# Optimization experiments

Hardware: AMD Instinct MI355X
Metric: run time of the kernel (lower is better)

## Reference

```python
import jax, jax.numpy as jnp
import numpy as np

C_S, C_Z, C_H = 384, 128, 128
EPS = 0.001      # norm-divisor eps (module's self.eps)
LN_EPS = 1e-5    # nn.LayerNorm default eps


def setup_inputs() -> dict:
    key = jax.random.key(0)
    ks = jax.random.split(key, 8)
    sc_in = 1.0 / np.sqrt(C_S)
    sc_out = 1.0 / np.sqrt(2 * C_H)
    return {
        "s1": jax.random.normal(ks[0], (1, 512, C_S), dtype=jnp.float32),
        "s2": jax.random.normal(ks[1], (1, 512, C_S), dtype=jnp.float32),
        "W1": jax.random.normal(ks[2], (C_H, C_S), dtype=jnp.float32) * sc_in,
        "b1": jnp.zeros((C_H,), dtype=jnp.float32),
        "W2": jax.random.normal(ks[3], (C_H, C_S), dtype=jnp.float32) * sc_in,
        "b2": jnp.zeros((C_H,), dtype=jnp.float32),
        "gamma": jnp.ones((C_H,), dtype=jnp.float32),
        "beta": jnp.zeros((C_H,), dtype=jnp.float32),
        "Wout": jax.random.normal(ks[4], (C_Z, 2 * C_H), dtype=jnp.float32) * sc_out,
        "bout": jnp.zeros((C_Z,), dtype=jnp.float32),
    }


def _layer_norm(x, gamma, beta):
    mu = jnp.mean(x, axis=-1, keepdims=True)
    var = jnp.mean(jnp.square(x - mu), axis=-1, keepdims=True)
    return (x - mu) * jax.lax.rsqrt(var + LN_EPS) * gamma + beta


def reference(s1, s2, W1, b1, W2, b2, gamma, beta, Wout, bout):
    # project + layernorm: [B, N, c_h], [B, M, c_h]
    a = _layer_norm(jnp.einsum('bns,hs->bnh', s1, W1) + b1, gamma, beta)
    b = _layer_norm(jnp.einsum('bms,hs->bmh', s2, W2) + b2, gamma, beta)
    n, m = a.shape[1], b.shape[1]
    # pairwise outer-concat: [B, N, M, 2*c_h]
    cmct = jnp.concatenate([
        jnp.broadcast_to(a[:, :, None, :], (a.shape[0], n, m, a.shape[-1])),
        jnp.broadcast_to(b[:, None, :, :], (b.shape[0], n, m, b.shape[-1])),
    ], axis=-1)
    cmct = cmct / (EPS + n * m)
    # linear out: [B, N, M, c_z]
    return jnp.einsum('bnmh,zh->bnmz', cmct, Wout) + bout
```

## Files before the change

### kernel.cpp

```cpp
#include <hip/hip_runtime.h>

#define C_S 384
#define C_H 128
#define NROWS 512
#define R 2

typedef float f4 __attribute__((ext_vector_type(4)));

__global__ __launch_bounds__(256, 4) void proj_ln_out(
    const float* __restrict__ s1, const float* __restrict__ s2,
    const float* __restrict__ W1, const float* __restrict__ b1,
    const float* __restrict__ W2, const float* __restrict__ b2,
    const float* __restrict__ gamma, const float* __restrict__ beta,
    const float* __restrict__ Wout, const float* __restrict__ bout,
    float* __restrict__ u, float* __restrict__ v)
{
    const int bid = blockIdx.x;
    const int nb_side = NROWS / R;
    const bool isA = bid < nb_side;
    const int r0 = (isA ? bid : bid - nb_side) * R;
    const float* __restrict__ src  = isA ? s1 : s2;
    const float* __restrict__ W    = isA ? W1 : W2;
    const float* __restrict__ bias = isA ? b1 : b2;
    float* __restrict__ dst = isA ? u : v;
    const int wout_off = isA ? 0 : C_H;

    const int tid  = threadIdx.x;
    const int wv   = tid >> 6;
    const int lane = tid & 63;
    const int g    = lane >> 4;
    const int j    = lane & 15;

    __shared__ __align__(16) float ylds[R][C_H];
    __shared__ __align__(16) float lnv[R][C_H];

    f4 sreg[R][6];
    #pragma unroll
    for (int r = 0; r < R; ++r) {
        const float* p = src + (r0 + r) * C_S + j * 24;
        #pragma unroll
        for (int q = 0; q < 6; ++q)
            sreg[r][q] = *reinterpret_cast<const f4*>(p + 4 * q);
    }

    for (int i = 0; i < 8; ++i) {
        const int h = wv * 32 + i * 4 + g;
        const float* wp = W + h * C_S + j * 24;
        f4 wr[6];
        #pragma unroll
        for (int q = 0; q < 6; ++q)
            wr[q] = *reinterpret_cast<const f4*>(wp + 4 * q);
        float acc[R];
        #pragma unroll
        for (int r = 0; r < R; ++r) {
            f4 a = wr[0] * sreg[r][0];
            #pragma unroll
            for (int q = 1; q < 6; ++q) a += wr[q] * sreg[r][q];
            acc[r] = (a.x + a.y) + (a.z + a.w);
        }
        #pragma unroll
        for (int off = 1; off < 16; off <<= 1)
            #pragma unroll
            for (int r = 0; r < R; ++r)
                acc[r] += __shfl_xor(acc[r], off);
        if (j == 0) {
            #pragma unroll
            for (int r = 0; r < R; ++r) ylds[r][h] = acc[r];
        }
    }
    __syncthreads();

    if (wv < R) {
        const int r = wv;
        const float y0 = ylds[r][lane]      + bias[lane];
        const float y1 = ylds[r][lane + 64] + bias[lane + 64];
        float s = y0 + y1, q = y0 * y0 + y1 * y1;
        #pragma unroll
        for (int off = 1; off < 64; off <<= 1) {
            s += __shfl_xor(s, off);
            q += __shfl_xor(q, off);
        }
        const float mu  = s * (1.0f / C_H);
        const float var = q * (1.0f / C_H) - mu * mu;
        const float rs  = rsqrtf(var + 1e-5f);
        lnv[r][lane]      = (y0 - mu) * rs * gamma[lane]      + beta[lane];
        lnv[r][lane + 64] = (y1 - mu) * rs * gamma[lane + 64] + beta[lane + 64];
    }
    __syncthreads();

    f4 lreg[R][2];
    #pragma unroll
    for (int r = 0; r < R; ++r) {
        lreg[r][0] = *reinterpret_cast<const f4*>(&lnv[r][j * 8]);
        lreg[r][1] = *reinterpret_cast<const f4*>(&lnv[r][j * 8 + 4]);
    }
    const float invD = (float)(1.0 / (0.001 + 262144.0));
    #pragma unroll 2
    for (int i = 0; i < 8; ++i) {
        const int zc = wv * 32 + i * 4 + g;
        const float* wp = Wout + zc * (2 * C_H) + wout_off + j * 8;
        const f4 w0 = *reinterpret_cast<const f4*>(wp);
        const f4 w1 = *reinterpret_cast<const f4*>(wp + 4);
        float acc[R];
        #pragma unroll
        for (int r = 0; r < R; ++r) {
            f4 a = w0 * lreg[r][0] + w1 * lreg[r][1];
            acc[r] = (a.x + a.y) + (a.z + a.w);
        }
        #pragma unroll
        for (int off = 1; off < 16; off <<= 1)
            #pragma unroll
            for (int r = 0; r < R; ++r)
                acc[r] += __shfl_xor(acc[r], off);
        if (j == 0) {
            #pragma unroll
            for (int r = 0; r < R; ++r)
                dst[(r0 + r) * C_H + zc] = acc[r] * invD + (isA ? bout[zc] : 0.f);
        }
    }
}

#define NTHREADS (2048 * 256)
__global__ __launch_bounds__(256) void bcast_add(
    const float* __restrict__ u, const float* __restrict__ v,
    float* __restrict__ out)
{
    const size_t tid = (size_t)blockIdx.x * 256 + threadIdx.x;
    const f4* __restrict__ uq = reinterpret_cast<const f4*>(u);
    f4* __restrict__ oq = reinterpret_cast<f4*>(out);
    const f4 v4 = reinterpret_cast<const f4*>(v)[tid & 16383];
    const int zq = (int)(tid & 31);
    #pragma unroll
    for (int k = 0; k < 16; ++k) {
        const size_t i = tid + (size_t)k * NTHREADS;
        const size_t un = i >> 14;
        const f4 o = uq[(un << 5) | zq] + v4;
        __builtin_nontemporal_store(o, &oq[i]);
    }
}

extern "C" void kernel_launch(void* const* d_in, const int* in_sizes, int n_in,
                              void* d_out, int out_size, void* d_ws, size_t ws_size,
                              hipStream_t stream) {
    const float* s1    = (const float*)d_in[0];
    const float* s2    = (const float*)d_in[1];
    const float* W1    = (const float*)d_in[2];
    const float* b1    = (const float*)d_in[3];
    const float* W2    = (const float*)d_in[4];
    const float* b2    = (const float*)d_in[5];
    const float* gamma = (const float*)d_in[6];
    const float* beta  = (const float*)d_in[7];
    const float* Wout  = (const float*)d_in[8];
    const float* bout  = (const float*)d_in[9];

    float* u = (float*)d_ws;
    float* v = u + NROWS * C_H;

    proj_ln_out<<<2 * (NROWS / R), 256, 0, stream>>>(s1, s2, W1, b1, W2, b2,
                                                     gamma, beta, Wout, bout, u, v);
    bcast_add<<<2048, 256, 0, stream>>>(u, v, (float*)d_out);
}
```

Measured before the change: 44.63 us.

## Fuse projection and broadcast-add kernels using an atomic grid barrier

```diff
diff --git a/kernel.cpp b/kernel.cpp
--- a/kernel.cpp
+++ b/kernel.cpp
@@ -7,13 +7,14 @@
 
 typedef float f4 __attribute__((ext_vector_type(4)));
 
-__global__ __launch_bounds__(256, 4) void proj_ln_out(
+__global__ __launch_bounds__(256) void fused_comm(
     const float* __restrict__ s1, const float* __restrict__ s2,
     const float* __restrict__ W1, const float* __restrict__ b1,
     const float* __restrict__ W2, const float* __restrict__ b2,
     const float* __restrict__ gamma, const float* __restrict__ beta,
     const float* __restrict__ Wout, const float* __restrict__ bout,
-    float* __restrict__ u, float* __restrict__ v)
+    float* __restrict__ u, float* __restrict__ v,
+    unsigned int* __restrict__ ctr, float* __restrict__ out)
 {
     const int bid = blockIdx.x;
     const int nb_side = NROWS / R;
@@ -118,24 +119,28 @@
                 dst[(r0 + r) * C_H + zc] = acc[r] * invD + (isA ? bout[zc] : 0.f);
         }
     }
-}
 
-#define NTHREADS (2048 * 256)
-__global__ __launch_bounds__(256) void bcast_add(
-    const float* __restrict__ u, const float* __restrict__ v,
-    float* __restrict__ out)
-{
-    const size_t tid = (size_t)blockIdx.x * 256 + threadIdx.x;
+    __threadfence();
+    __syncthreads();
+    if (tid == 0) {
+        atomicAdd(ctr, 1u);
+        while (atomicAdd(ctr, 0u) < (unsigned)(2 * nb_side))
+            __builtin_amdgcn_s_sleep(2);
+    }
+    __syncthreads();
+    __threadfence();
+
+    const int n  = bid;
+    const int zq = tid & 31;
+    const int ml = tid >> 5;
     const f4* __restrict__ uq = reinterpret_cast<const f4*>(u);
-    f4* __restrict__ oq = reinterpret_cast<f4*>(out);
-    const f4 v4 = reinterpret_cast<const f4*>(v)[tid & 16383];
-    const int zq = (int)(tid & 31);
-    #pragma unroll
-    for (int k = 0; k < 16; ++k) {
-        const size_t i = tid + (size_t)k * NTHREADS;
-        const size_t un = i >> 14;
-        const f4 o = uq[(un << 5) | zq] + v4;
-        __builtin_nontemporal_store(o, &oq[i]);
+    const f4* __restrict__ vq = reinterpret_cast<const f4*>(v);
+    f4* __restrict__ oq = reinterpret_cast<f4*>(out) + (size_t)n * 16384;
+    const f4 u4 = uq[n * 32 + zq];
+    #pragma unroll 4
+    for (int it = 0; it < 64; ++it) {
+        const int m = it * 8 + ml;
+        oq[(size_t)m * 32 + zq] = u4 + vq[m * 32 + zq];
     }
 }
 
@@ -155,8 +160,10 @@
 
     float* u = (float*)d_ws;
     float* v = u + NROWS * C_H;
+    unsigned int* ctr = (unsigned int*)(v + NROWS * C_H);
 
-    proj_ln_out<<<2 * (NROWS / R), 256, 0, stream>>>(s1, s2, W1, b1, W2, b2,
-                                                     gamma, beta, Wout, bout, u, v);
-    bcast_add<<<2048, 256, 0, stream>>>(u, v, (float*)d_out);
+    hipMemsetAsync(ctr, 0, sizeof(unsigned int), stream);
+    fused_comm<<<2 * NROWS / R, 256, 0, stream>>>(s1, s2, W1, b1, W2, b2,
+                                                  gamma, beta, Wout, bout,
+                                                  u, v, ctr, (float*)d_out);
 }
```

Result: slower. 127.7 us (+186.0%).
